# Kernel tuning notes

Measured on AMD Instinct MI355X. Metric: run time of the kernel, lower is better.

The kernel has to match this reference:

```python
import jax, jax.numpy as jnp
import numpy as np

EC = 256   # ec
CT = 512   # ct
NH = 8     # heads
K = 3      # adaptive pool output
HC = EC // NH
CH = (256, 512, 1024)
HW = (48, 24, 12)
BS = 32
NT = 512   # number of text queries


def _ln(x, g, b, eps=1e-5):
    m = jnp.mean(x, axis=-1, keepdims=True)
    v = jnp.mean((x - m) ** 2, axis=-1, keepdims=True)
    return (x - m) * jax.lax.rsqrt(v + eps) * g + b


def _adaptive_max_pool(x, k):
    # H, W divisible by k -> uniform bins, identical to AdaptiveMaxPool2d
    B, C, H, W = x.shape
    return x.reshape(B, C, k, H // k, k, W // k).max(axis=(3, 5))


def setup_inputs() -> dict:
    key = jax.random.key(0)
    ks = jax.random.split(key, 32)
    d = {}
    for i, (c, s) in enumerate(zip(CH, HW)):
        d[f"x{i}"] = jax.random.normal(ks[i], (BS, c, s, s), jnp.float32)
    d["text"] = jax.random.normal(ks[3], (BS, NT, CT), jnp.float32)
    # 1x1 conv projections (stored as [C_in, EC] matrices)
    for i, c in enumerate(CH):
        d[f"w{i}"] = jax.random.normal(ks[4 + i], (c, EC), jnp.float32) / np.sqrt(c).astype(np.float32)
        d[f"cb{i}"] = jax.random.normal(ks[7 + i], (EC,), jnp.float32) * 0.02
    # LayerNorm + Linear for query (ct->ec), key/value (ec->ec)
    d["q_ln_g"] = jnp.ones((CT,), jnp.float32); d["q_ln_b"] = jnp.zeros((CT,), jnp.float32)
    d["k_ln_g"] = jnp.ones((EC,), jnp.float32); d["k_ln_b"] = jnp.zeros((EC,), jnp.float32)
    d["v_ln_g"] = jnp.ones((EC,), jnp.float32); d["v_ln_b"] = jnp.zeros((EC,), jnp.float32)
    d["q_w"] = jax.random.normal(ks[10], (CT, EC), jnp.float32) / np.sqrt(CT).astype(np.float32)
    d["q_b"] = jax.random.normal(ks[11], (EC,), jnp.float32) * 0.02
    d["k_w"] = jax.random.normal(ks[12], (EC, EC), jnp.float32) / np.sqrt(EC).astype(np.float32)
    d["k_b"] = jax.random.normal(ks[13], (EC,), jnp.float32) * 0.02
    d["v_w"] = jax.random.normal(ks[14], (EC, EC), jnp.float32) / np.sqrt(EC).astype(np.float32)
    d["v_b"] = jax.random.normal(ks[15], (EC,), jnp.float32) * 0.02
    d["proj_w"] = jax.random.normal(ks[16], (EC, CT), jnp.float32) / np.sqrt(EC).astype(np.float32)
    d["proj_b"] = jax.random.normal(ks[17], (CT,), jnp.float32) * 0.02
    return d


def reference(x0, x1, x2, text, w0, cb0, w1, cb1, w2, cb2,
              q_ln_g, q_ln_b, k_ln_g, k_ln_b, v_ln_g, v_ln_b,
              q_w, q_b, k_w, k_b, v_w, v_b, proj_w, proj_b):
    bs = x0.shape[0]
    feats = []
    for x, w, b in ((x0, w0, cb0), (x1, w1, cb1), (x2, w2, cb2)):
        p = jnp.einsum('bchw,ce->behw', x, w) + b[None, :, None, None]  # 1x1 conv
        feats.append(_adaptive_max_pool(p, K).reshape(bs, EC, K * K))
    xc = jnp.concatenate(feats, axis=-1).transpose(0, 2, 1)  # (bs, 27, ec)

    q = _ln(text, q_ln_g, q_ln_b) @ q_w + q_b   # (bs, NT, ec)
    k = _ln(xc, k_ln_g, k_ln_b) @ k_w + k_b     # (bs, 27, ec)
    v = _ln(xc, v_ln_g, v_ln_b) @ v_w + v_b     # (bs, 27, ec)

    q = q.reshape(bs, -1, NH, HC)
    k = k.reshape(bs, -1, NH, HC)
    v = v.reshape(bs, -1, NH, HC)

    aw = jnp.einsum('bnmc,bkmc->bmnk', q, k) / np.sqrt(HC).astype(np.float32)
    aw = jax.nn.softmax(aw, axis=-1)
    o = jnp.einsum('bmnk,bkmc->bnmc', aw, v).reshape(bs, -1, EC)
    return o @ proj_w + proj_b + text  # scale=False -> scale == 1.0
```

## Files before the change

kernel.cpp:

```cpp
#include <hip/hip_runtime.h>
#include <stdint.h>

#define DEVFN __device__ __forceinline__

using f32x4   = __attribute__((ext_vector_type(4)))  float;
using f32x8   = __attribute__((ext_vector_type(8)))  float;
using f32x16  = __attribute__((ext_vector_type(16))) float;
using us4     = __attribute__((ext_vector_type(4)))  unsigned short;
using us8     = __attribute__((ext_vector_type(8)))  unsigned short;
using u32x4   = __attribute__((ext_vector_type(4)))  unsigned int;
using bf16x8  = __attribute__((ext_vector_type(8)))  __bf16;

DEVFN unsigned short f2b(float x){
    union { float f; unsigned u; } v; v.f = x;
    unsigned r = v.u + 0x7FFFu + ((v.u >> 16) & 1u);
    return (unsigned short)(r >> 16);
}
DEVFN float b2f(unsigned short u){
    union { unsigned u; float f; } v; v.u = ((unsigned)u) << 16; return v.f;
}
DEVFN bf16x8 ld_bf16x8(const unsigned short* p){
    return __builtin_bit_cast(bf16x8, *(const us8*)p);
}
DEVFN bf16x8 pack_bf16x8v(f32x8 f){
    us8 u;
#pragma unroll
    for (int j = 0; j < 8; ++j) u[j] = f2b(f[j]);
    return __builtin_bit_cast(bf16x8, u);
}
DEVFN f32x16 zero16(){
    f32x16 z;
#pragma unroll
    for (int i = 0; i < 16; ++i) z[i] = 0.f;
    return z;
}
DEVFN f32x16 mfma_bf16(bf16x8 a, bf16x8 b, f32x16 c){
    return __builtin_amdgcn_mfma_f32_32x32x16_bf16(a, b, c, 0, 0, 0);
}
DEVFN void gload_lds16(const unsigned short* g, unsigned short* l){
    __builtin_amdgcn_global_load_lds(
        (const __attribute__((address_space(1))) unsigned int*)(const void*)g,
        (__attribute__((address_space(3))) unsigned int*)(void*)l,
        16, 0, 0);
}
template<int HW>
DEVFN f32x8 loadA8(const float* ap){
    f32x8 v;
#pragma unroll
    for (int j = 0; j < 8; ++j) v[j] = ap[(size_t)j * HW];
    return v;
}

__global__ __launch_bounds__(256) void k_prep(
        const float* __restrict__ w0, const float* __restrict__ w1,
        const float* __restrict__ w2, const float* __restrict__ qw,
        const float* __restrict__ pw, const float* __restrict__ kw,
        const float* __restrict__ vw,
        unsigned short* __restrict__ o0, unsigned short* __restrict__ o1,
        unsigned short* __restrict__ o2, unsigned short* __restrict__ oq,
        unsigned short* __restrict__ op, unsigned short* __restrict__ ok,
        unsigned short* __restrict__ ov){
    int gid = blockIdx.x * 256 + threadIdx.x;
    const float* in; unsigned short* out; int t, E;
    if (gid < 8192)       { in = w0; out = o0; t = gid;         E = 256; }
    else if (gid < 24576) { in = w1; out = o1; t = gid - 8192;  E = 256; }
    else if (gid < 57344) { in = w2; out = o2; t = gid - 24576; E = 256; }
    else if (gid < 73728) { in = qw; out = oq; t = gid - 57344; E = 256; }
    else if (gid < 90112) { in = pw; out = op; t = gid - 73728; E = 512; }
    else if (gid < 98304) { in = kw; out = ok; t = gid - 90112; E = 256; }
    else                  { in = vw; out = ov; t = gid - 98304; E = 256; }
    int lane = t & 63, fn = t >> 6;
    int nt, ks;
    if (E == 512){ nt = fn & 15; ks = fn >> 4; }
    else         { nt = fn & 7;  ks = fn >> 3; }
    int c0 = ks*16 + (lane >> 5)*8, e = nt*32 + (lane & 31);
    us8 u;
#pragma unroll
    for (int j = 0; j < 8; ++j) u[j] = f2b(in[(size_t)(c0 + j) * E + e]);
    *(us8*)(out + (size_t)t * 8) = u;
}

DEVFN void comp4(f32x16 (&acc)[8], f32x8 a, const unsigned short* bsmr, int kk, int lane){
    bf16x8 A = pack_bf16x8v(a);
#pragma unroll
    for (int nt = 0; nt < 8; ++nt){
        bf16x8 B = ld_bf16x8(bsmr + (kk*8 + nt) * 512 + lane * 8);
        acc[nt] = mfma_bf16(A, B, acc[nt]);
    }
}

template<int C, int WIMG, int BINW>
DEVFN void conv_sub(const float* __restrict__ X, const unsigned short* __restrict__ WF,
                    unsigned short* bsm0, unsigned short* bsm1,
                    int b, int bin, int sub, float* rmax){
    const int HW = WIMG * WIMG;
    const int NCH = C / 32;
    int w = threadIdx.x >> 6, lane = threadIdx.x & 63, lo = lane & 31, hi = lane >> 5;
    int binr = bin / 3, binc = bin % 3;
    int prow, pcol;
    if constexpr (BINW == 16){ prow = sub*2 + (lo>>4); pcol = lo & 15; }
    else if constexpr (BINW == 8){ prow = sub*4 + (lo>>3); pcol = lo & 7; }
    else { prow = (lo & 15) >> 2; pcol = lo & 3; }
    int gr = binr * BINW + prow, gc = binc * BINW + pcol;
    const float* Xk = X + (size_t)b * C * HW + gr * WIMG + gc + (size_t)hi * 8 * HW;

    f32x16 acc[8];
#pragma unroll
    for (int nt = 0; nt < 8; ++nt) acc[nt] = zero16();

    auto stage = [&](unsigned short* dst, int ch){
        const unsigned short* src = WF + (size_t)ch * 8192 + w * 2048 + lane * 8;
        unsigned short* dl = dst + w * 2048;
#pragma unroll
        for (int it = 0; it < 4; ++it)
            gload_lds16(src + it * 512, dl + it * 512);
    };

    __syncthreads();
    stage(bsm0, 0);
    f32x8 a0 = loadA8<HW>(Xk);
    f32x8 a1 = loadA8<HW>(Xk + (size_t)16 * HW);
    __syncthreads();

    unsigned short* cur = bsm0;
    unsigned short* nxt = bsm1;
    for (int c = 0; c < NCH; ++c){
        f32x8 p0, p1;
        bool more = (c + 1 < NCH);
        if (more){
            stage(nxt, c + 1);
            const float* Xn = Xk + (size_t)(c + 1) * 32 * HW;
            p0 = loadA8<HW>(Xn);
            p1 = loadA8<HW>(Xn + (size_t)16 * HW);
        }
        comp4(acc, a0, cur, 0, lane);
        comp4(acc, a1, cur, 1, lane);
        __syncthreads();
        if (more){ a0 = p0; a1 = p1; }
        unsigned short* t = cur; cur = nxt; nxt = t;
    }
#pragma unroll
    for (int nt = 0; nt < 8; ++nt){
        float m = acc[nt][0];
#pragma unroll
        for (int r = 1; r < 16; ++r) m = fmaxf(m, acc[nt][r]);
        rmax[nt] = fmaxf(rmax[nt], m);
    }
}

__global__ __launch_bounds__(256, 1) void k_conv_pool(
        const float* __restrict__ x0, const float* __restrict__ x1, const float* __restrict__ x2,
        const unsigned short* __restrict__ wt0, const unsigned short* __restrict__ wt1,
        const unsigned short* __restrict__ wt2,
        const float* __restrict__ cb0, const float* __restrict__ cb1, const float* __restrict__ cb2,
        float* __restrict__ xc){
    __shared__ __attribute__((aligned(16))) unsigned short bsm0[8192];
    __shared__ __attribute__((aligned(16))) unsigned short bsm1[8192];
    __shared__ float red[4][8][32];
    int blk = blockIdx.x, w = threadIdx.x >> 6, lane = threadIdx.x & 63;
    int lo = lane & 31, hi = lane >> 5;
    float rmax[8];
#pragma unroll
    for (int nt = 0; nt < 8; ++nt) rmax[nt] = -3.4e38f;

    if (blk < 96){
        int r = blk, b = r / 3, q = r % 3;
        int bin = q*4 + w;
        int bc = bin <= 8 ? bin : 8;
        conv_sub<1024, 12, 4>(x2, wt2, bsm0, bsm1, b, bc, 0, rmax);
#pragma unroll
        for (int nt = 0; nt < 8; ++nt){
            float m = fmaxf(rmax[nt], __shfl_xor(rmax[nt], 32));
            if (hi == 0 && bin <= 8){
                int e = nt*32 + lo;
                xc[((size_t)b*27 + 18 + bin)*256 + e] = m + cb2[e];
            }
        }
    } else if (blk < 256){
        int r = blk - 96, b = r / 5, p = r % 5;
        int binA = 2*p;
        bool hasB = (2*p + 1 <= 8);
        int binB = hasB ? 2*p + 1 : binA;
        int bin = (w < 2) ? binA : binB;
        conv_sub<512, 24, 8>(x1, wt1, bsm0, bsm1, b, bin, w & 1, rmax);
#pragma unroll
        for (int nt = 0; nt < 8; ++nt){
            float m = fmaxf(rmax[nt], __shfl_xor(rmax[nt], 32));
            if (hi == 0) red[w][nt][lo] = m;
        }
        __syncthreads();
        int t = threadIdx.x, nt = t >> 5, l = t & 31, e = nt*32 + l;
        float mA = fmaxf(red[0][nt][l], red[1][nt][l]);
        xc[((size_t)b*27 + 9 + binA)*256 + e] = mA + cb1[e];
        if (hasB){
            float mB = fmaxf(red[2][nt][l], red[3][nt][l]);
            xc[((size_t)b*27 + 9 + binB)*256 + e] = mB + cb1[e];
        }
    } else {
        int r = blk - 256, b = r / 9, bin = r % 9;
        conv_sub<256, 48, 16>(x0, wt0, bsm0, bsm1, b, bin, w,     rmax);
        conv_sub<256, 48, 16>(x0, wt0, bsm0, bsm1, b, bin, w + 4, rmax);
#pragma unroll
        for (int nt = 0; nt < 8; ++nt){
            float m = fmaxf(rmax[nt], __shfl_xor(rmax[nt], 32));
            if (hi == 0) red[w][nt][lo] = m;
        }
        __syncthreads();
        int t = threadIdx.x, nt = t >> 5, l = t & 31, e = nt*32 + l;
        float m = fmaxf(fmaxf(red[0][nt][l], red[1][nt][l]),
                        fmaxf(red[2][nt][l], red[3][nt][l]));
        xc[((size_t)b*27 + bin)*256 + e] = m + cb0[e];
    }
}

__global__ __launch_bounds__(128) void k_lnq(const float* __restrict__ text,
        const float* __restrict__ g, const float* __restrict__ bb,
        const unsigned short* __restrict__ qwt, const float* __restrict__ qb,
        unsigned short* __restrict__ qout){
    __shared__ unsigned short alds[32][520];
    int w = threadIdx.x >> 6, lane = threadIdx.x & 63, lo = lane & 31, hi = lane >> 5;
    size_t row0 = (size_t)blockIdx.x * 32;

    const float* gp = g  + lane * 8;
    const float* bp = bb + lane * 8;
    f32x4 g0 = *(const f32x4*)gp, g1 = *(const f32x4*)(gp+4);
    f32x4 b0 = *(const f32x4*)bp, b1 = *(const f32x4*)(bp+4);
#pragma unroll
    for (int it = 0; it < 16; ++it){
        int r = it * 2 + w;
        const float* p = text + (row0 + r) * 512 + lane * 8;
        f32x4 a = *(const f32x4*)p;
        f32x4 c = *(const f32x4*)(p + 4);
        float s = a[0]+a[1]+a[2]+a[3]+c[0]+c[1]+c[2]+c[3];
#pragma unroll
        for (int off = 32; off; off >>= 1) s += __shfl_xor(s, off);
        float mean = s * (1.f/512.f);
        float d[8];
        d[0]=a[0]-mean; d[1]=a[1]-mean; d[2]=a[2]-mean; d[3]=a[3]-mean;
        d[4]=c[0]-mean; d[5]=c[1]-mean; d[6]=c[2]-mean; d[7]=c[3]-mean;
        float vs = d[0]*d[0]+d[1]*d[1]+d[2]*d[2]+d[3]*d[3]+d[4]*d[4]+d[5]*d[5]+d[6]*d[6]+d[7]*d[7];
#pragma unroll
        for (int off = 32; off; off >>= 1) vs += __shfl_xor(vs, off);
        float rstd = rsqrtf(vs * (1.f/512.f) + 1e-5f);
        us8 o;
#pragma unroll
        for (int j = 0; j < 4; ++j) o[j]   = f2b(d[j]  *rstd*g0[j] + b0[j]);
#pragma unroll
        for (int j = 0; j < 4; ++j) o[4+j] = f2b(d[4+j]*rstd*g1[j] + b1[j]);
        *(us8*)(&alds[r][lane * 8]) = o;
    }
    __syncthreads();

    f32x16 acc[4];
#pragma unroll
    for (int i = 0; i < 4; ++i) acc[i] = zero16();
    const unsigned short* wf = qwt + (size_t)lane * 8;
    for (int ks = 0; ks < 32; ++ks){
        bf16x8 a = ld_bf16x8(&alds[lo][ks*16 + hi*8]);
#pragma unroll
        for (int i = 0; i < 4; ++i){
            int nt = w*4 + i;
            bf16x8 bfr = ld_bf16x8(wf + (size_t)(ks*8 + nt) * 512);
            acc[i] = mfma_bf16(a, bfr, acc[i]);
        }
    }
#pragma unroll
    for (int i = 0; i < 4; ++i){
        int e = (w*4 + i) * 32 + lo;
        float qbias = qb[e];
#pragma unroll
        for (int r = 0; r < 16; ++r){
            size_t row = row0 + (r & 3) + 8 * (r >> 2) + 4 * hi;
            qout[row * 256 + e] = f2b(acc[i][r] + qbias);
        }
    }
}

__global__ __launch_bounds__(256) void k_kv(const float* __restrict__ xc,
        const float* __restrict__ kg, const float* __restrict__ kb,
        const float* __restrict__ vg, const float* __restrict__ vb,
        const unsigned short* __restrict__ kwt, const unsigned short* __restrict__ vwt,
        const float* __restrict__ k_bias, const float* __restrict__ v_bias,
        float* __restrict__ kout, float* __restrict__ vout){
    __shared__ unsigned short lnk[32][264];
    __shared__ unsigned short lnv[32][264];
    int w = threadIdx.x >> 6, lane = threadIdx.x & 63, lo = lane & 31, hi = lane >> 5;
    size_t row0 = (size_t)blockIdx.x * 32;
    int c0 = lane * 4;
    f32x4 kgv = *(const f32x4*)(kg + c0), kbv = *(const f32x4*)(kb + c0);
    f32x4 vgv = *(const f32x4*)(vg + c0), vbv = *(const f32x4*)(vb + c0);
#pragma unroll
    for (int rr = 0; rr < 8; ++rr){
        int r = w * 8 + rr;
        f32x4 xv = *(const f32x4*)(xc + (row0 + r) * 256 + c0);
        float s = xv[0]+xv[1]+xv[2]+xv[3];
#pragma unroll
        for (int off = 32; off; off >>= 1) s += __shfl_xor(s, off);
        float mean = s * (1.f/256.f);
        float d0 = xv[0]-mean, d1 = xv[1]-mean, d2 = xv[2]-mean, d3 = xv[3]-mean;
        float vs = d0*d0 + d1*d1 + d2*d2 + d3*d3;
#pragma unroll
        for (int off = 32; off; off >>= 1) vs += __shfl_xor(vs, off);
        float rstd = rsqrtf(vs * (1.f/256.f) + 1e-5f);
        us4 uk, uv;
        uk[0] = f2b(d0*rstd*kgv[0] + kbv[0]); uv[0] = f2b(d0*rstd*vgv[0] + vbv[0]);
        uk[1] = f2b(d1*rstd*kgv[1] + kbv[1]); uv[1] = f2b(d1*rstd*vgv[1] + vbv[1]);
        uk[2] = f2b(d2*rstd*kgv[2] + kbv[2]); uv[2] = f2b(d2*rstd*vgv[2] + vbv[2]);
        uk[3] = f2b(d3*rstd*kgv[3] + kbv[3]); uv[3] = f2b(d3*rstd*vgv[3] + vbv[3]);
        *(us4*)(&lnk[r][c0]) = uk;
        *(us4*)(&lnv[r][c0]) = uv;
    }
    __syncthreads();

    f32x16 acc[4];
#pragma unroll
    for (int i = 0; i < 4; ++i) acc[i] = zero16();
    const unsigned short* lds = (w < 2) ? &lnk[0][0] : &lnv[0][0];
    const unsigned short* wf  = ((w < 2) ? kwt : vwt) + (size_t)lane * 8;
    int ntb = (w & 1) * 4;
    for (int ks = 0; ks < 16; ++ks){
        bf16x8 a = ld_bf16x8(lds + lo*264 + ks*16 + hi*8);
#pragma unroll
        for (int i = 0; i < 4; ++i){
            int nt = ntb + i;
            bf16x8 bfr = ld_bf16x8(wf + (size_t)(ks*8 + nt) * 512);
            acc[i] = mfma_bf16(a, bfr, acc[i]);
        }
    }
    const float* bias = (w < 2) ? k_bias : v_bias;
    float* outp = (w < 2) ? kout : vout;
#pragma unroll
    for (int i = 0; i < 4; ++i){
        int e = (ntb + i) * 32 + lo;
        float bv = bias[e];
#pragma unroll
        for (int r = 0; r < 16; ++r){
            size_t row = row0 + (r & 3) + 8 * (r >> 2) + 4 * hi;
            outp[row * 256 + e] = acc[i][r] + bv;
        }
    }
}

__global__ __launch_bounds__(256, 3) void k_attnproj(const unsigned short* __restrict__ qbf,
        const float* __restrict__ kbuf, const float* __restrict__ vbuf,
        const unsigned short* __restrict__ pwt, const float* __restrict__ pb,
        const float* __restrict__ text, float* __restrict__ out){
    int b = blockIdx.x >> 4;
    int rg = blockIdx.x & 15;
    __shared__ unsigned short klds[32][264];
    __shared__ unsigned short vT[256][36];
    __shared__ unsigned short qolds[32][264];
    int tid = threadIdx.x;
    int w = tid >> 6, lane = tid & 63, lo = lane & 31, hi = lane >> 5;
    size_t grow0 = (size_t)b * 512 + rg * 32;

    for (int i = tid; i < 27 * 64; i += 256){
        int row = i >> 6, c4 = (i & 63) << 2;
        f32x4 kv = *(const f32x4*)(kbuf + ((size_t)b*27 + row) * 256 + c4);
        us4 u; u[0]=f2b(kv[0]); u[1]=f2b(kv[1]); u[2]=f2b(kv[2]); u[3]=f2b(kv[3]);
        *(us4*)(&klds[row][c4]) = u;
    }
    for (int i = tid; i < 330; i += 256){
        int row = 27 + i / 66, c4 = (i % 66) * 4;
        us4 z = {0,0,0,0};
        *(us4*)(&klds[row][c4]) = z;
    }
    {
        int ch = tid;
        for (int k = 0; k < 27; ++k)
            vT[ch][k] = f2b(vbuf[((size_t)b*27 + k) * 256 + ch]);
#pragma unroll
        for (int k = 27; k < 36; ++k) vT[ch][k] = 0;
    }
    for (int i = tid; i < 1024; i += 256){
        int row = i >> 5, c8 = (i & 31) << 3;
        *(us8*)(&qolds[row][c8]) = *(const us8*)(qbf + (grow0 + row) * 256 + c8);
    }
    __syncthreads();

#pragma unroll
    for (int hh = 0; hh < 2; ++hh){
        int h = w + hh * 4;
        int hc = h * 32;
        f32x16 s = zero16();
        {
            bf16x8 A0 = ld_bf16x8(&klds[lo][hc + hi*8]);
            bf16x8 B0 = ld_bf16x8(&qolds[lo][hc + hi*8]);
            s = mfma_bf16(A0, B0, s);
            bf16x8 A1 = ld_bf16x8(&klds[lo][hc + 16 + hi*8]);
            bf16x8 B1 = ld_bf16x8(&qolds[lo][hc + 16 + hi*8]);
            s = mfma_bf16(A1, B1, s);
        }
        float mx = -3.4e38f;
#pragma unroll
        for (int r = 0; r < 16; ++r){
            bool valid = hi ? (r < 12) : (r != 15);
            if (valid) mx = fmaxf(mx, s[r]);
        }
        mx = fmaxf(mx, __shfl_xor(mx, 32));
        float p[16]; float sum = 0.f;
#pragma unroll
        for (int r = 0; r < 16; ++r){
            bool valid = hi ? (r < 12) : (r != 15);
            p[r] = valid ? __expf((s[r] - mx) * 0.17677669529663687f) : 0.f;
            sum += p[r];
        }
        sum += __shfl_xor(sum, 32);
        float inv = 1.f / sum;
        unsigned pd[8];
#pragma unroll
        for (int i = 0; i < 8; ++i)
            pd[i] = (unsigned)f2b(p[2*i]*inv) | ((unsigned)f2b(p[2*i+1]*inv) << 16);

        f32x16 o = zero16();
#pragma unroll
        for (int c = 0; c < 2; ++c){
            unsigned own0 = hi ? pd[4*c+2] : pd[4*c];
            unsigned own1 = hi ? pd[4*c+3] : pd[4*c+1];
            unsigned snd0 = hi ? pd[4*c]   : pd[4*c+2];
            unsigned snd1 = hi ? pd[4*c+1] : pd[4*c+3];
            unsigned rcv0 = (unsigned)__shfl_xor((int)snd0, 32);
            unsigned rcv1 = (unsigned)__shfl_xor((int)snd1, 32);
            u32x4 bd;
            bd[0] = hi ? rcv0 : own0;
            bd[1] = hi ? rcv1 : own1;
            bd[2] = hi ? own0 : rcv0;
            bd[3] = hi ? own1 : rcv1;
            bf16x8 B = __builtin_bit_cast(bf16x8, bd);
            bf16x8 A = ld_bf16x8(&vT[hc + lo][c*16 + hi*8]);
            o = mfma_bf16(A, B, o);
        }
#pragma unroll
        for (int g = 0; g < 4; ++g){
            us4 u;
#pragma unroll
            for (int j = 0; j < 4; ++j) u[j] = f2b(o[g*4 + j]);
            *(us4*)(&qolds[lo][hc + g*8 + hi*4]) = u;
        }
    }
    __syncthreads();

    f32x16 acc[4];
#pragma unroll
    for (int i = 0; i < 4; ++i) acc[i] = zero16();
    const unsigned short* wf = pwt + (size_t)lane * 8;
    for (int ks = 0; ks < 16; ++ks){
        bf16x8 a = ld_bf16x8(&qolds[lo][ks*16 + hi*8]);
#pragma unroll
        for (int i = 0; i < 4; ++i){
            int nt = w*4 + i;
            bf16x8 bfr = ld_bf16x8(wf + (size_t)(ks*16 + nt) * 512);
            acc[i] = mfma_bf16(a, bfr, acc[i]);
        }
    }
#pragma unroll
    for (int i = 0; i < 4; ++i){
        int ct = (w*4 + i) * 32 + lo;
        float pbias = pb[ct];
#pragma unroll
        for (int r = 0; r < 16; ++r){
            size_t row = grow0 + (r & 3) + 8 * (r >> 2) + 4 * hi;
            out[row * 512 + ct] = acc[i][r] + pbias + text[row * 512 + ct];
        }
    }
}

extern "C" void kernel_launch(void* const* d_in, const int* in_sizes, int n_in,
                              void* d_out, int out_size, void* d_ws, size_t ws_size,
                              hipStream_t stream) {
    (void)in_sizes; (void)n_in; (void)out_size; (void)ws_size;
    const float* x0     = (const float*)d_in[0];
    const float* x1     = (const float*)d_in[1];
    const float* x2     = (const float*)d_in[2];
    const float* text   = (const float*)d_in[3];
    const float* w0     = (const float*)d_in[4];
    const float* cb0    = (const float*)d_in[5];
    const float* w1     = (const float*)d_in[6];
    const float* cb1    = (const float*)d_in[7];
    const float* w2     = (const float*)d_in[8];
    const float* cb2    = (const float*)d_in[9];
    const float* q_ln_g = (const float*)d_in[10];
    const float* q_ln_b = (const float*)d_in[11];
    const float* k_ln_g = (const float*)d_in[12];
    const float* k_ln_b = (const float*)d_in[13];
    const float* v_ln_g = (const float*)d_in[14];
    const float* v_ln_b = (const float*)d_in[15];
    const float* q_w    = (const float*)d_in[16];
    const float* q_b    = (const float*)d_in[17];
    const float* k_w    = (const float*)d_in[18];
    const float* k_b    = (const float*)d_in[19];
    const float* v_w    = (const float*)d_in[20];
    const float* v_b    = (const float*)d_in[21];
    const float* proj_w = (const float*)d_in[22];
    const float* proj_b = (const float*)d_in[23];
    float* out = (float*)d_out;

    char* wsb = (char*)d_ws; size_t off = 0;
    auto take = [&](size_t bytes) -> void* {
        void* p = wsb + off; off += (bytes + 255) & ~(size_t)255; return p;
    };
    unsigned short* qbf    = (unsigned short*)take((size_t)16384 * 256 * 2);
    float*          xc     = (float*)take((size_t)32 * 27 * 256 * 4);
    float*          kbuf   = (float*)take((size_t)32 * 27 * 256 * 4);
    float*          vbuf   = (float*)take((size_t)32 * 27 * 256 * 4);
    unsigned short* wt0    = (unsigned short*)take((size_t)256 * 256 * 2);
    unsigned short* wt1    = (unsigned short*)take((size_t)256 * 512 * 2);
    unsigned short* wt2    = (unsigned short*)take((size_t)256 * 1024 * 2);
    unsigned short* qwt    = (unsigned short*)take((size_t)256 * 512 * 2);
    unsigned short* pwt    = (unsigned short*)take((size_t)512 * 256 * 2);
    unsigned short* kwt    = (unsigned short*)take((size_t)256 * 256 * 2);
    unsigned short* vwt    = (unsigned short*)take((size_t)256 * 256 * 2);

    k_prep<<<416, 256, 0, stream>>>(w0, w1, w2, q_w, proj_w, k_w, v_w,
                                    wt0, wt1, wt2, qwt, pwt, kwt, vwt);
    k_conv_pool<<<544, 256, 0, stream>>>(x0, x1, x2, wt0, wt1, wt2, cb0, cb1, cb2, xc);
    k_lnq<<<512, 128, 0, stream>>>(text, q_ln_g, q_ln_b, qwt, q_b, qbf);
    k_kv<<<27, 256, 0, stream>>>(xc, k_ln_g, k_ln_b, v_ln_g, v_ln_b,
                                 kwt, vwt, k_b, v_b, kbuf, vbuf);
    k_attnproj<<<512, 256, 0, stream>>>(qbf, kbuf, vbuf, pwt, proj_b, text, out);
}
```

Baseline: 148.9 us.

## Split conv-pool output channels across two wave groups with 512-thread blocks

The conv+maxpool kernel now launches 512 threads per block. Each wave handles half of the 256 output channels (4 MFMA n-tiles instead of 8), and the two halves of the block share the staged weight tiles. This halves the accumulator registers per wave and doubles the waves available to hide the global A-loads, with the aim of better latency hiding and occupancy. The cost is that every LDS weight tile and every A-operand load is now shared or duplicated across twice as many waves, and the final cross-wave reduction has to be reorganised to match.

Result: faster. 145.9 us (-2.0%).

```diff
diff --git a/kernel.cpp b/kernel.cpp
--- a/kernel.cpp
+++ b/kernel.cpp
@@ -80,22 +80,22 @@
     *(us8*)(out + (size_t)t * 8) = u;
 }
 
-DEVFN void comp4(f32x16 (&acc)[8], f32x8 a, const unsigned short* bsmr, int kk, int lane){
+DEVFN void comp2(f32x16 (&acc)[4], f32x8 a, const unsigned short* bsmr, int kk, int ntb, int lane){
     bf16x8 A = pack_bf16x8v(a);
 #pragma unroll
-    for (int nt = 0; nt < 8; ++nt){
-        bf16x8 B = ld_bf16x8(bsmr + (kk*8 + nt) * 512 + lane * 8);
-        acc[nt] = mfma_bf16(A, B, acc[nt]);
+    for (int i = 0; i < 4; ++i){
+        bf16x8 B = ld_bf16x8(bsmr + (kk*8 + ntb + i) * 512 + lane * 8);
+        acc[i] = mfma_bf16(A, B, acc[i]);
     }
 }
 
 template<int C, int WIMG, int BINW>
 DEVFN void conv_sub(const float* __restrict__ X, const unsigned short* __restrict__ WF,
                     unsigned short* bsm0, unsigned short* bsm1,
-                    int b, int bin, int sub, float* rmax){
+                    int b, int bin, int sub, int ntb, float* rmax){
     const int HW = WIMG * WIMG;
     const int NCH = C / 32;
-    int w = threadIdx.x >> 6, lane = threadIdx.x & 63, lo = lane & 31, hi = lane >> 5;
+    int w8 = threadIdx.x >> 6, lane = threadIdx.x & 63, lo = lane & 31, hi = lane >> 5;
     int binr = bin / 3, binc = bin % 3;
     int prow, pcol;
     if constexpr (BINW == 16){ prow = sub*2 + (lo>>4); pcol = lo & 15; }
@@ -104,16 +104,15 @@
     int gr = binr * BINW + prow, gc = binc * BINW + pcol;
     const float* Xk = X + (size_t)b * C * HW + gr * WIMG + gc + (size_t)hi * 8 * HW;
 
-    f32x16 acc[8];
-#pragma unroll
-    for (int nt = 0; nt < 8; ++nt) acc[nt] = zero16();
+    f32x16 acc[4];
+#pragma unroll
+    for (int i = 0; i < 4; ++i) acc[i] = zero16();
 
     auto stage = [&](unsigned short* dst, int ch){
-        const unsigned short* src = WF + (size_t)ch * 8192 + w * 2048 + lane * 8;
-        unsigned short* dl = dst + w * 2048;
-#pragma unroll
-        for (int it = 0; it < 4; ++it)
-            gload_lds16(src + it * 512, dl + it * 512);
+        const unsigned short* src = WF + (size_t)ch * 8192 + w8 * 1024 + lane * 8;
+        unsigned short* dl = dst + w8 * 1024;
+        gload_lds16(src,       dl);
+        gload_lds16(src + 512, dl + 512);
     };
 
     __syncthreads();
@@ -133,22 +132,22 @@
             p0 = loadA8<HW>(Xn);
             p1 = loadA8<HW>(Xn + (size_t)16 * HW);
         }
-        comp4(acc, a0, cur, 0, lane);
-        comp4(acc, a1, cur, 1, lane);
+        comp2(acc, a0, cur, 0, ntb, lane);
+        comp2(acc, a1, cur, 1, ntb, lane);
         __syncthreads();
         if (more){ a0 = p0; a1 = p1; }
         unsigned short* t = cur; cur = nxt; nxt = t;
     }
 #pragma unroll
-    for (int nt = 0; nt < 8; ++nt){
-        float m = acc[nt][0];
-#pragma unroll
-        for (int r = 1; r < 16; ++r) m = fmaxf(m, acc[nt][r]);
-        rmax[nt] = fmaxf(rmax[nt], m);
-    }
-}
-
-__global__ __launch_bounds__(256, 1) void k_conv_pool(
+    for (int i = 0; i < 4; ++i){
+        float m = acc[i][0];
+#pragma unroll
+        for (int r = 1; r < 16; ++r) m = fmaxf(m, acc[i][r]);
+        rmax[i] = fmaxf(rmax[i], m);
+    }
+}
+
+__global__ __launch_bounds__(512, 4) void k_conv_pool(
         const float* __restrict__ x0, const float* __restrict__ x1, const float* __restrict__ x2,
         const unsigned short* __restrict__ wt0, const unsigned short* __restrict__ wt1,
         const unsigned short* __restrict__ wt2,
@@ -156,23 +155,24 @@
         float* __restrict__ xc){
     __shared__ __attribute__((aligned(16))) unsigned short bsm0[8192];
     __shared__ __attribute__((aligned(16))) unsigned short bsm1[8192];
-    __shared__ float red[4][8][32];
+    __shared__ float red[8][4][32];
     int blk = blockIdx.x, w = threadIdx.x >> 6, lane = threadIdx.x & 63;
     int lo = lane & 31, hi = lane >> 5;
-    float rmax[8];
-#pragma unroll
-    for (int nt = 0; nt < 8; ++nt) rmax[nt] = -3.4e38f;
+    int ntb = (w >> 2) * 4;
+    float rmax[4];
+#pragma unroll
+    for (int i = 0; i < 4; ++i) rmax[i] = -3.4e38f;
 
     if (blk < 96){
-        int r = blk, b = r / 3, q = r % 3;
-        int bin = q*4 + w;
+        int b = blk / 3, q = blk % 3;
+        int bin = q*4 + (w & 3);
         int bc = bin <= 8 ? bin : 8;
-        conv_sub<1024, 12, 4>(x2, wt2, bsm0, bsm1, b, bc, 0, rmax);
-#pragma unroll
-        for (int nt = 0; nt < 8; ++nt){
-            float m = fmaxf(rmax[nt], __shfl_xor(rmax[nt], 32));
+        conv_sub<1024, 12, 4>(x2, wt2, bsm0, bsm1, b, bc, 0, ntb, rmax);
+#pragma unroll
+        for (int i = 0; i < 4; ++i){
+            float m = fmaxf(rmax[i], __shfl_xor(rmax[i], 32));
             if (hi == 0 && bin <= 8){
-                int e = nt*32 + lo;
+                int e = (ntb + i)*32 + lo;
                 xc[((size_t)b*27 + 18 + bin)*256 + e] = m + cb2[e];
             }
         }
@@ -181,35 +181,40 @@
         int binA = 2*p;
         bool hasB = (2*p + 1 <= 8);
         int binB = hasB ? 2*p + 1 : binA;
-        int bin = (w < 2) ? binA : binB;
-        conv_sub<512, 24, 8>(x1, wt1, bsm0, bsm1, b, bin, w & 1, rmax);
-#pragma unroll
-        for (int nt = 0; nt < 8; ++nt){
-            float m = fmaxf(rmax[nt], __shfl_xor(rmax[nt], 32));
-            if (hi == 0) red[w][nt][lo] = m;
+        int bin = ((w >> 1) & 1) ? binB : binA;
+        conv_sub<512, 24, 8>(x1, wt1, bsm0, bsm1, b, bin, w & 1, ntb, rmax);
+#pragma unroll
+        for (int i = 0; i < 4; ++i){
+            float m = fmaxf(rmax[i], __shfl_xor(rmax[i], 32));
+            if (hi == 0) red[w][i][lo] = m;
         }
         __syncthreads();
-        int t = threadIdx.x, nt = t >> 5, l = t & 31, e = nt*32 + l;
-        float mA = fmaxf(red[0][nt][l], red[1][nt][l]);
-        xc[((size_t)b*27 + 9 + binA)*256 + e] = mA + cb1[e];
-        if (hasB){
-            float mB = fmaxf(red[2][nt][l], red[3][nt][l]);
-            xc[((size_t)b*27 + 9 + binB)*256 + e] = mB + cb1[e];
-        }
+        int t = threadIdx.x;
+        int binIdx = t >> 8, e = t & 255;
+        int half = e >> 7, ntl = (e >> 5) & 3, l = e & 31;
+        int w0 = half*4 + binIdx*2;
+        float m = fmaxf(red[w0][ntl][l], red[w0+1][ntl][l]);
+        if (binIdx == 0)      xc[((size_t)b*27 + 9 + binA)*256 + e] = m + cb1[e];
+        else if (hasB)        xc[((size_t)b*27 + 9 + binB)*256 + e] = m + cb1[e];
     } else {
         int r = blk - 256, b = r / 9, bin = r % 9;
-        conv_sub<256, 48, 16>(x0, wt0, bsm0, bsm1, b, bin, w,     rmax);
-        conv_sub<256, 48, 16>(x0, wt0, bsm0, bsm1, b, bin, w + 4, rmax);
-#pragma unroll
-        for (int nt = 0; nt < 8; ++nt){
-            float m = fmaxf(rmax[nt], __shfl_xor(rmax[nt], 32));
-            if (hi == 0) red[w][nt][lo] = m;
+        int s0i = w & 3;
+        conv_sub<256, 48, 16>(x0, wt0, bsm0, bsm1, b, bin, s0i,     ntb, rmax);
+        conv_sub<256, 48, 16>(x0, wt0, bsm0, bsm1, b, bin, s0i + 4, ntb, rmax);
+#pragma unroll
+        for (int i = 0; i < 4; ++i){
+            float m = fmaxf(rmax[i], __shfl_xor(rmax[i], 32));
+            if (hi == 0) red[w][i][lo] = m;
         }
         __syncthreads();
-        int t = threadIdx.x, nt = t >> 5, l = t & 31, e = nt*32 + l;
-        float m = fmaxf(fmaxf(red[0][nt][l], red[1][nt][l]),
-                        fmaxf(red[2][nt][l], red[3][nt][l]));
-        xc[((size_t)b*27 + bin)*256 + e] = m + cb0[e];
+        int t = threadIdx.x;
+        if (t < 256){
+            int e = t, half = e >> 7, ntl = (e >> 5) & 3, l = e & 31;
+            int wb = half * 4;
+            float m = fmaxf(fmaxf(red[wb][ntl][l], red[wb+1][ntl][l]),
+                            fmaxf(red[wb+2][ntl][l], red[wb+3][ntl][l]));
+            xc[((size_t)b*27 + bin)*256 + e] = m + cb0[e];
+        }
     }
 }
 
@@ -513,7 +518,7 @@
 
     k_prep<<<416, 256, 0, stream>>>(w0, w1, w2, q_w, proj_w, k_w, v_w,
                                     wt0, wt1, wt2, qwt, pwt, kwt, vwt);
-    k_conv_pool<<<544, 256, 0, stream>>>(x0, x1, x2, wt0, wt1, wt2, cb0, cb1, cb2, xc);
+    k_conv_pool<<<544, 512, 0, stream>>>(x0, x1, x2, wt0, wt1, wt2, cb0, cb1, cb2, xc);
     k_lnq<<<512, 128, 0, stream>>>(text, q_ln_g, q_ln_b, qwt, q_b, qbf);
     k_kv<<<27, 256, 0, stream>>>(xc, k_ln_g, k_ln_b, v_ln_g, v_ln_b,
                                  kwt, vwt, k_b, v_b, kbuf, vbuf);
```

## Split conv-pool work across independent waves, dropping LDS weight staging

Applied to the files above, without the earlier changes.

The fused 1x1-conv plus adaptive max-pool kernel is restructured so each wave owns one (batch, bin, quarter of output channels) task and reads bf16 weights straight from global memory. This removes the LDS double-buffered weight staging, block-level barriers and shared-memory reductions. Occupancy goes up through launch_bounds(256,4) and a larger grid. In exchange, each input activation column is now loaded four times, once per channel-quarter wave, and weight reads rely on cache rather than shared memory.

Measured after the change: 167.1 us. +12.2%, slower.

```diff
diff --git a/kernel.cpp b/kernel.cpp
--- a/kernel.cpp
+++ b/kernel.cpp
@@ -36,12 +36,6 @@
 }
 DEVFN f32x16 mfma_bf16(bf16x8 a, bf16x8 b, f32x16 c){
     return __builtin_amdgcn_mfma_f32_32x32x16_bf16(a, b, c, 0, 0, 0);
-}
-DEVFN void gload_lds16(const unsigned short* g, unsigned short* l){
-    __builtin_amdgcn_global_load_lds(
-        (const __attribute__((address_space(1))) unsigned int*)(const void*)g,
-        (__attribute__((address_space(3))) unsigned int*)(void*)l,
-        16, 0, 0);
 }
 template<int HW>
 DEVFN f32x8 loadA8(const float* ap){
@@ -80,136 +74,72 @@
     *(us8*)(out + (size_t)t * 8) = u;
 }
 
-DEVFN void comp4(f32x16 (&acc)[8], f32x8 a, const unsigned short* bsmr, int kk, int lane){
-    bf16x8 A = pack_bf16x8v(a);
-#pragma unroll
-    for (int nt = 0; nt < 8; ++nt){
-        bf16x8 B = ld_bf16x8(bsmr + (kk*8 + nt) * 512 + lane * 8);
-        acc[nt] = mfma_bf16(A, B, acc[nt]);
-    }
-}
-
-template<int C, int WIMG, int BINW>
-DEVFN void conv_sub(const float* __restrict__ X, const unsigned short* __restrict__ WF,
-                    unsigned short* bsm0, unsigned short* bsm1,
-                    int b, int bin, int sub, float* rmax){
+template<int C, int WIMG, int BINW, int NSUB>
+DEVFN void conv_wave(const float* __restrict__ X, const unsigned short* __restrict__ WF,
+                     const float* __restrict__ CB, float* __restrict__ xc,
+                     int b, int bin, int eq, int sbase){
     const int HW = WIMG * WIMG;
-    const int NCH = C / 32;
-    int w = threadIdx.x >> 6, lane = threadIdx.x & 63, lo = lane & 31, hi = lane >> 5;
+    const int NK = C / 16;
+    int lane = threadIdx.x & 63, lo = lane & 31, hi = lane >> 5;
     int binr = bin / 3, binc = bin % 3;
-    int prow, pcol;
-    if constexpr (BINW == 16){ prow = sub*2 + (lo>>4); pcol = lo & 15; }
-    else if constexpr (BINW == 8){ prow = sub*4 + (lo>>3); pcol = lo & 7; }
-    else { prow = (lo & 15) >> 2; pcol = lo & 3; }
-    int gr = binr * BINW + prow, gc = binc * BINW + pcol;
-    const float* Xk = X + (size_t)b * C * HW + gr * WIMG + gc + (size_t)hi * 8 * HW;
-
-    f32x16 acc[8];
-#pragma unroll
-    for (int nt = 0; nt < 8; ++nt) acc[nt] = zero16();
-
-    auto stage = [&](unsigned short* dst, int ch){
-        const unsigned short* src = WF + (size_t)ch * 8192 + w * 2048 + lane * 8;
-        unsigned short* dl = dst + w * 2048;
-#pragma unroll
-        for (int it = 0; it < 4; ++it)
-            gload_lds16(src + it * 512, dl + it * 512);
-    };
-
-    __syncthreads();
-    stage(bsm0, 0);
-    f32x8 a0 = loadA8<HW>(Xk);
-    f32x8 a1 = loadA8<HW>(Xk + (size_t)16 * HW);
-    __syncthreads();
-
-    unsigned short* cur = bsm0;
-    unsigned short* nxt = bsm1;
-    for (int c = 0; c < NCH; ++c){
-        f32x8 p0, p1;
-        bool more = (c + 1 < NCH);
-        if (more){
-            stage(nxt, c + 1);
-            const float* Xn = Xk + (size_t)(c + 1) * 32 * HW;
-            p0 = loadA8<HW>(Xn);
-            p1 = loadA8<HW>(Xn + (size_t)16 * HW);
-        }
-        comp4(acc, a0, cur, 0, lane);
-        comp4(acc, a1, cur, 1, lane);
-        __syncthreads();
-        if (more){ a0 = p0; a1 = p1; }
-        unsigned short* t = cur; cur = nxt; nxt = t;
-    }
-#pragma unroll
-    for (int nt = 0; nt < 8; ++nt){
-        float m = acc[nt][0];
-#pragma unroll
-        for (int r = 1; r < 16; ++r) m = fmaxf(m, acc[nt][r]);
-        rmax[nt] = fmaxf(rmax[nt], m);
-    }
-}
-
-__global__ __launch_bounds__(256, 1) void k_conv_pool(
+    const unsigned short* wf = WF + (size_t)lane * 8;
+    int nt0 = eq * 2, nt1 = eq * 2 + 1;
+    float rmax0 = -3.4e38f, rmax1 = -3.4e38f;
+
+    for (int sub = 0; sub < NSUB; ++sub){
+        int prow, pcol;
+        if constexpr (BINW == 16){ prow = sub*2 + (lo>>4); pcol = lo & 15; }
+        else if constexpr (BINW == 8){ prow = sub*4 + (lo>>3); pcol = lo & 7; }
+        else { prow = (lo & 15) >> 2; pcol = lo & 3; }
+        int gr = binr * BINW + prow, gc = binc * BINW + pcol;
+        const float* Xp = X + (size_t)b * C * HW + gr * WIMG + gc + (size_t)hi * 8 * HW;
+
+        f32x16 a0 = zero16(), a1 = zero16();
+        f32x8 aC = loadA8<HW>(Xp);
+        f32x8 aN = loadA8<HW>(Xp + (size_t)16 * HW);
+        for (int ks = 0; ks < NK; ++ks){
+            f32x8 aF;
+            if (ks + 2 < NK) aF = loadA8<HW>(Xp + (size_t)(ks + 2) * 16 * HW);
+            bf16x8 B0 = ld_bf16x8(wf + (size_t)(ks*8 + nt0) * 512);
+            bf16x8 B1 = ld_bf16x8(wf + (size_t)(ks*8 + nt1) * 512);
+            bf16x8 A = pack_bf16x8v(aC);
+            a0 = mfma_bf16(A, B0, a0);
+            a1 = mfma_bf16(A, B1, a1);
+            aC = aN;
+            if (ks + 2 < NK) aN = aF;
+        }
+        float m0 = a0[0], m1 = a1[0];
+#pragma unroll
+        for (int r = 1; r < 16; ++r){ m0 = fmaxf(m0, a0[r]); m1 = fmaxf(m1, a1[r]); }
+        rmax0 = fmaxf(rmax0, m0);
+        rmax1 = fmaxf(rmax1, m1);
+    }
+    rmax0 = fmaxf(rmax0, __shfl_xor(rmax0, 32));
+    rmax1 = fmaxf(rmax1, __shfl_xor(rmax1, 32));
+    if (hi == 0){
+        size_t base = ((size_t)b * 27 + sbase + bin) * 256;
+        int e0 = nt0 * 32 + lo, e1 = nt1 * 32 + lo;
+        xc[base + e0] = rmax0 + CB[e0];
+        xc[base + e1] = rmax1 + CB[e1];
+    }
+}
+
+__global__ __launch_bounds__(256, 4) void k_conv_pool(
         const float* __restrict__ x0, const float* __restrict__ x1, const float* __restrict__ x2,
         const unsigned short* __restrict__ wt0, const unsigned short* __restrict__ wt1,
         const unsigned short* __restrict__ wt2,
         const float* __restrict__ cb0, const float* __restrict__ cb1, const float* __restrict__ cb2,
         float* __restrict__ xc){
-    __shared__ __attribute__((aligned(16))) unsigned short bsm0[8192];
-    __shared__ __attribute__((aligned(16))) unsigned short bsm1[8192];
-    __shared__ float red[4][8][32];
-    int blk = blockIdx.x, w = threadIdx.x >> 6, lane = threadIdx.x & 63;
-    int lo = lane & 31, hi = lane >> 5;
-    float rmax[8];
-#pragma unroll
-    for (int nt = 0; nt < 8; ++nt) rmax[nt] = -3.4e38f;
-
-    if (blk < 96){
-        int r = blk, b = r / 3, q = r % 3;
-        int bin = q*4 + w;
-        int bc = bin <= 8 ? bin : 8;
-        conv_sub<1024, 12, 4>(x2, wt2, bsm0, bsm1, b, bc, 0, rmax);
-#pragma unroll
-        for (int nt = 0; nt < 8; ++nt){
-            float m = fmaxf(rmax[nt], __shfl_xor(rmax[nt], 32));
-            if (hi == 0 && bin <= 8){
-                int e = nt*32 + lo;
-                xc[((size_t)b*27 + 18 + bin)*256 + e] = m + cb2[e];
-            }
-        }
-    } else if (blk < 256){
-        int r = blk - 96, b = r / 5, p = r % 5;
-        int binA = 2*p;
-        bool hasB = (2*p + 1 <= 8);
-        int binB = hasB ? 2*p + 1 : binA;
-        int bin = (w < 2) ? binA : binB;
-        conv_sub<512, 24, 8>(x1, wt1, bsm0, bsm1, b, bin, w & 1, rmax);
-#pragma unroll
-        for (int nt = 0; nt < 8; ++nt){
-            float m = fmaxf(rmax[nt], __shfl_xor(rmax[nt], 32));
-            if (hi == 0) red[w][nt][lo] = m;
-        }
-        __syncthreads();
-        int t = threadIdx.x, nt = t >> 5, l = t & 31, e = nt*32 + l;
-        float mA = fmaxf(red[0][nt][l], red[1][nt][l]);
-        xc[((size_t)b*27 + 9 + binA)*256 + e] = mA + cb1[e];
-        if (hasB){
-            float mB = fmaxf(red[2][nt][l], red[3][nt][l]);
-            xc[((size_t)b*27 + 9 + binB)*256 + e] = mB + cb1[e];
-        }
+    int task = blockIdx.x * 4 + (threadIdx.x >> 6);
+    if (task < 1152){
+        int r = task; int eq = r & 3; r >>= 2; int bin = r % 9, b = r / 9;
+        conv_wave<256, 48, 16, 8>(x0, wt0, cb0, xc, b, bin, eq, 0);
+    } else if (task < 2304){
+        int r = task - 1152; int eq = r & 3; r >>= 2; int bin = r % 9, b = r / 9;
+        conv_wave<512, 24, 8, 2>(x1, wt1, cb1, xc, b, bin, eq, 9);
     } else {
-        int r = blk - 256, b = r / 9, bin = r % 9;
-        conv_sub<256, 48, 16>(x0, wt0, bsm0, bsm1, b, bin, w,     rmax);
-        conv_sub<256, 48, 16>(x0, wt0, bsm0, bsm1, b, bin, w + 4, rmax);
-#pragma unroll
-        for (int nt = 0; nt < 8; ++nt){
-            float m = fmaxf(rmax[nt], __shfl_xor(rmax[nt], 32));
-            if (hi == 0) red[w][nt][lo] = m;
-        }
-        __syncthreads();
-        int t = threadIdx.x, nt = t >> 5, l = t & 31, e = nt*32 + l;
-        float m = fmaxf(fmaxf(red[0][nt][l], red[1][nt][l]),
-                        fmaxf(red[2][nt][l], red[3][nt][l]));
-        xc[((size_t)b*27 + bin)*256 + e] = m + cb0[e];
+        int r = task - 2304; int eq = r & 3; r >>= 2; int bin = r % 9, b = r / 9;
+        conv_wave<1024, 12, 4, 1>(x2, wt2, cb2, xc, b, bin, eq, 18);
     }
 }
 
@@ -513,7 +443,7 @@
 
     k_prep<<<416, 256, 0, stream>>>(w0, w1, w2, q_w, proj_w, k_w, v_w,
                                     wt0, wt1, wt2, qwt, pwt, kwt, vwt);
-    k_conv_pool<<<544, 256, 0, stream>>>(x0, x1, x2, wt0, wt1, wt2, cb0, cb1, cb2, xc);
+    k_conv_pool<<<864, 256, 0, stream>>>(x0, x1, x2, wt0, wt1, wt2, cb0, cb1, cb2, xc);
     k_lnq<<<512, 128, 0, stream>>>(text, q_ln_g, q_ln_b, qwt, q_b, qbf);
     k_kv<<<27, 256, 0, stream>>>(xc, k_ln_g, k_ln_b, v_ln_g, v_ln_b,
                                  kwt, vwt, k_b, v_b, kbuf, vbuf);
```
